# Performance work log

Hardware: AMD Instinct MI355X
Metric: run time of the kernel (lower is better)

## Reference

```python
import jax, jax.numpy as jnp
import numpy as np

STATE = 65536
INPUT = 32768
CONCAT = STATE + INPUT
H1, H2 = 100, 50
NGATES = 4  # forget, input, cell, output


def setup_inputs() -> dict:
    key = jax.random.key(0)
    ks = jax.random.split(key, 9)
    s = lambda n: 1.0 / np.sqrt(n)
    return {
        "cell_state_prev": jax.random.normal(ks[0], (STATE,), jnp.float32),
        "hypotesis": jax.random.normal(ks[1], (STATE,), jnp.float32),
        "x": jax.random.normal(ks[2], (INPUT,), jnp.float32),
        # stacked per-gate MLP params: gate order [forget, input, cell, output]
        "W1": jax.random.uniform(ks[3], (NGATES, H1, CONCAT), jnp.float32, -s(CONCAT), s(CONCAT)),
        "b1": jax.random.uniform(ks[4], (NGATES, H1), jnp.float32, -s(CONCAT), s(CONCAT)),
        "W2": jax.random.uniform(ks[5], (NGATES, H2, H1), jnp.float32, -s(H1), s(H1)),
        "b2": jax.random.uniform(ks[6], (NGATES, H2), jnp.float32, -s(H1), s(H1)),
        "W3": jax.random.uniform(ks[7], (NGATES, STATE, H2), jnp.float32, -s(H2), s(H2)),
        "b3": jax.random.uniform(ks[8], (NGATES, STATE), jnp.float32, -s(H2), s(H2)),
    }


def reference(cell_state_prev, hypotesis, x, W1, b1, W2, b2, W3, b3):
    c = jnp.concatenate([hypotesis, x])                     # [CONCAT]
    h1 = jax.nn.relu(jnp.einsum('ghc,c->gh', W1, c) + b1)   # [4, 100]
    h2 = jax.nn.relu(jnp.einsum('gkh,gh->gk', W2, h1) + b2) # [4, 50]
    z = jnp.einsum('gsk,gk->gs', W3, h2) + b3               # [4, STATE]
    forget_gate = jax.nn.sigmoid(z[0])
    input_gate = jax.nn.sigmoid(z[1])
    cell_state_hat = jnp.tanh(z[2])
    output_gate = jax.nn.sigmoid(z[3])
    new_cell_state = forget_gate * cell_state_prev + input_gate * cell_state_hat
    new_hypotesis = jnp.tanh(new_cell_state) * output_gate
    return (new_hypotesis, new_cell_state)
```

## Files before the change

kernel.cpp:

```cpp
#include <hip/hip_runtime.h>
#include <math.h>

#define STATE  65536
#define INPUT  32768
#define CONCAT 98304
#define H1_    100
#define H2_    50
#define NG     4

__global__ __launch_bounds__(1024) void k1_h1(
    const float* __restrict__ hyp, const float* __restrict__ x,
    const float* __restrict__ W1,  const float* __restrict__ b1,
    float* __restrict__ h1)
{
    const int row = blockIdx.x;
    const int tid = threadIdx.x;
    const float* __restrict__ Wrow = W1 + (size_t)row * CONCAT;

    float4 acc = make_float4(0.f, 0.f, 0.f, 0.f);

    #pragma unroll
    for (int it = 0; it < 16; ++it) {
        const int i = it * 4096 + tid * 4;
        const float4 w = *reinterpret_cast<const float4*>(Wrow + i);
        const float4 v = *reinterpret_cast<const float4*>(hyp + i);
        acc.x = fmaf(w.x, v.x, acc.x);
        acc.y = fmaf(w.y, v.y, acc.y);
        acc.z = fmaf(w.z, v.z, acc.z);
        acc.w = fmaf(w.w, v.w, acc.w);
    }
    #pragma unroll
    for (int it = 0; it < 8; ++it) {
        const int i = it * 4096 + tid * 4;
        const float4 w = *reinterpret_cast<const float4*>(Wrow + STATE + i);
        const float4 v = *reinterpret_cast<const float4*>(x + i);
        acc.x = fmaf(w.x, v.x, acc.x);
        acc.y = fmaf(w.y, v.y, acc.y);
        acc.z = fmaf(w.z, v.z, acc.z);
        acc.w = fmaf(w.w, v.w, acc.w);
    }

    float sum = (acc.x + acc.y) + (acc.z + acc.w);

    #pragma unroll
    for (int off = 32; off > 0; off >>= 1)
        sum += __shfl_down(sum, off, 64);

    __shared__ float wsum[16];
    if ((tid & 63) == 0) wsum[tid >> 6] = sum;
    __syncthreads();

    if (tid < 16) {
        float s = wsum[tid];
        s += __shfl_down(s, 8, 64);
        s += __shfl_down(s, 4, 64);
        s += __shfl_down(s, 2, 64);
        s += __shfl_down(s, 1, 64);
        if (tid == 0) h1[row] = fmaxf(s + b1[row], 0.f);
    }
}

__global__ __launch_bounds__(256) void k3_out(
    const float* __restrict__ h1, const float* __restrict__ W2,
    const float* __restrict__ b2, const float* __restrict__ W3,
    const float* __restrict__ b3, const float* __restrict__ cprev,
    float* __restrict__ out)
{
    __shared__ float h1s[NG * H1_];
    __shared__ float h2s[NG * H2_];
    __shared__ float zsh[NG * 64];

    const int tid = threadIdx.x;

    for (int i = tid; i < NG * H1_; i += 256) h1s[i] = h1[i];
    __syncthreads();

    if (tid < NG * H2_) {
        const int g = tid / H2_;
        const float* __restrict__ Wr = W2 + tid * H1_;
        float4 a = make_float4(0.f, 0.f, 0.f, 0.f);
        #pragma unroll
        for (int j = 0; j < H1_ / 4; ++j) {
            const float4 w = *reinterpret_cast<const float4*>(Wr + 4 * j);
            a.x = fmaf(w.x, h1s[g * H1_ + 4 * j + 0], a.x);
            a.y = fmaf(w.y, h1s[g * H1_ + 4 * j + 1], a.y);
            a.z = fmaf(w.z, h1s[g * H1_ + 4 * j + 2], a.z);
            a.w = fmaf(w.w, h1s[g * H1_ + 4 * j + 3], a.w);
        }
        const float v = (a.x + a.y) + (a.z + a.w) + b2[tid];
        h2s[tid] = fmaxf(v, 0.f);
    }
    __syncthreads();

    const int g    = tid >> 6;
    const int lane = tid & 63;
    const int s    = blockIdx.x * 64 + lane;
    const float* __restrict__ Wr = W3 + ((size_t)g * STATE + s) * H2_;
    float a0 = 0.f, a1 = 0.f;
    #pragma unroll
    for (int k = 0; k < H2_; k += 2) {
        const float2 w = *reinterpret_cast<const float2*>(Wr + k);
        a0 = fmaf(w.x, h2s[g * H2_ + k + 0], a0);
        a1 = fmaf(w.y, h2s[g * H2_ + k + 1], a1);
    }
    zsh[g * 64 + lane] = a0 + a1 + b3[(size_t)g * STATE + s];
    __syncthreads();

    if (tid < 64) {
        const int ss = blockIdx.x * 64 + tid;
        const float zf = zsh[0 * 64 + tid];
        const float zi = zsh[1 * 64 + tid];
        const float zc = zsh[2 * 64 + tid];
        const float zo = zsh[3 * 64 + tid];
        const float fg = 1.f / (1.f + expf(-zf));
        const float ig = 1.f / (1.f + expf(-zi));
        const float ch = tanhf(zc);
        const float og = 1.f / (1.f + expf(-zo));
        const float nc = fg * cprev[ss] + ig * ch;
        const float nh = tanhf(nc) * og;
        out[ss]         = nh;
        out[STATE + ss] = nc;
    }
}

extern "C" void kernel_launch(void* const* d_in, const int* in_sizes, int n_in,
                              void* d_out, int out_size, void* d_ws, size_t ws_size,
                              hipStream_t stream) {
    const float* cprev = (const float*)d_in[0];
    const float* hyp   = (const float*)d_in[1];
    const float* x     = (const float*)d_in[2];
    const float* W1    = (const float*)d_in[3];
    const float* b1    = (const float*)d_in[4];
    const float* W2    = (const float*)d_in[5];
    const float* b2    = (const float*)d_in[6];
    const float* W3    = (const float*)d_in[7];
    const float* b3    = (const float*)d_in[8];
    float* out = (float*)d_out;
    float* h1  = (float*)d_ws;

    k1_h1<<<NG * H1_, 1024, 0, stream>>>(hyp, x, W1, b1, h1);
    k3_out<<<STATE / 64, 256, 0, stream>>>(h1, W2, b2, W3, b3, cprev, out);
}
```

Before: 294.2 us.

## Split W1 GEMV rows into column segments with partial sums reduced downstream

```diff
diff --git a/kernel.cpp b/kernel.cpp
--- a/kernel.cpp
+++ b/kernel.cpp
@@ -1,78 +1,71 @@
 #include <hip/hip_runtime.h>
 #include <math.h>
 
-#define STATE  65536
-#define INPUT  32768
-#define CONCAT 98304
-#define H1_    100
-#define H2_    50
-#define NG     4
+#define STATE   65536
+#define INPUT   32768
+#define CONCAT  98304
+#define H1_     100
+#define H2_     50
+#define NG      4
+#define NROWS   (NG * H1_)
+#define SEGS    6
+#define SEGCOLS 16384
 
-__global__ __launch_bounds__(1024) void k1_h1(
+__global__ __launch_bounds__(256) void k1_partial(
     const float* __restrict__ hyp, const float* __restrict__ x,
-    const float* __restrict__ W1,  const float* __restrict__ b1,
-    float* __restrict__ h1)
+    const float* __restrict__ W1,  float* __restrict__ part)
 {
-    const int row = blockIdx.x;
+    const int bid = blockIdx.x;
+    const int seg = bid / NROWS;
+    const int row = bid - seg * NROWS;
     const int tid = threadIdx.x;
-    const float* __restrict__ Wrow = W1 + (size_t)row * CONCAT;
+
+    const float* __restrict__ vec =
+        (seg < 4) ? (hyp + seg * SEGCOLS) : (x + (seg - 4) * SEGCOLS);
+    const float* __restrict__ w = W1 + (size_t)row * CONCAT + seg * SEGCOLS;
 
     float4 acc = make_float4(0.f, 0.f, 0.f, 0.f);
-
     #pragma unroll
     for (int it = 0; it < 16; ++it) {
-        const int i = it * 4096 + tid * 4;
-        const float4 w = *reinterpret_cast<const float4*>(Wrow + i);
-        const float4 v = *reinterpret_cast<const float4*>(hyp + i);
-        acc.x = fmaf(w.x, v.x, acc.x);
-        acc.y = fmaf(w.y, v.y, acc.y);
-        acc.z = fmaf(w.z, v.z, acc.z);
-        acc.w = fmaf(w.w, v.w, acc.w);
+        const int i = it * 1024 + tid * 4;
+        const float4 wv = *reinterpret_cast<const float4*>(w + i);
+        const float4 vv = *reinterpret_cast<const float4*>(vec + i);
+        acc.x = fmaf(wv.x, vv.x, acc.x);
+        acc.y = fmaf(wv.y, vv.y, acc.y);
+        acc.z = fmaf(wv.z, vv.z, acc.z);
+        acc.w = fmaf(wv.w, vv.w, acc.w);
     }
-    #pragma unroll
-    for (int it = 0; it < 8; ++it) {
-        const int i = it * 4096 + tid * 4;
-        const float4 w = *reinterpret_cast<const float4*>(Wrow + STATE + i);
-        const float4 v = *reinterpret_cast<const float4*>(x + i);
-        acc.x = fmaf(w.x, v.x, acc.x);
-        acc.y = fmaf(w.y, v.y, acc.y);
-        acc.z = fmaf(w.z, v.z, acc.z);
-        acc.w = fmaf(w.w, v.w, acc.w);
-    }
-
     float sum = (acc.x + acc.y) + (acc.z + acc.w);
 
     #pragma unroll
     for (int off = 32; off > 0; off >>= 1)
         sum += __shfl_down(sum, off, 64);
 
-    __shared__ float wsum[16];
+    __shared__ float wsum[4];
     if ((tid & 63) == 0) wsum[tid >> 6] = sum;
     __syncthreads();
-
-    if (tid < 16) {
-        float s = wsum[tid];
-        s += __shfl_down(s, 8, 64);
-        s += __shfl_down(s, 4, 64);
-        s += __shfl_down(s, 2, 64);
-        s += __shfl_down(s, 1, 64);
-        if (tid == 0) h1[row] = fmaxf(s + b1[row], 0.f);
-    }
+    if (tid == 0)
+        part[bid] = (wsum[0] + wsum[1]) + (wsum[2] + wsum[3]);
 }
 
 __global__ __launch_bounds__(256) void k3_out(
-    const float* __restrict__ h1, const float* __restrict__ W2,
-    const float* __restrict__ b2, const float* __restrict__ W3,
-    const float* __restrict__ b3, const float* __restrict__ cprev,
-    float* __restrict__ out)
+    const float* __restrict__ part, const float* __restrict__ b1,
+    const float* __restrict__ W2,   const float* __restrict__ b2,
+    const float* __restrict__ W3,   const float* __restrict__ b3,
+    const float* __restrict__ cprev, float* __restrict__ out)
 {
-    __shared__ float h1s[NG * H1_];
+    __shared__ float h1s[NROWS];
     __shared__ float h2s[NG * H2_];
     __shared__ float zsh[NG * 64];
 
     const int tid = threadIdx.x;
 
-    for (int i = tid; i < NG * H1_; i += 256) h1s[i] = h1[i];
+    for (int i = tid; i < NROWS; i += 256) {
+        float s = b1[i];
+        #pragma unroll
+        for (int seg = 0; seg < SEGS; ++seg) s += part[seg * NROWS + i];
+        h1s[i] = fmaxf(s, 0.f);
+    }
     __syncthreads();
 
     if (tid < NG * H2_) {
@@ -135,9 +128,9 @@
     const float* b2    = (const float*)d_in[6];
     const float* W3    = (const float*)d_in[7];
     const float* b3    = (const float*)d_in[8];
-    float* out = (float*)d_out;
-    float* h1  = (float*)d_ws;
+    float* out  = (float*)d_out;
+    float* part = (float*)d_ws;
 
-    k1_h1<<<NG * H1_, 1024, 0, stream>>>(hyp, x, W1, b1, h1);
-    k3_out<<<STATE / 64, 256, 0, stream>>>(h1, W2, b2, W3, b3, cprev, out);
+    k1_partial<<<SEGS * NROWS, 256, 0, stream>>>(hyp, x, W1, part);
+    k3_out<<<STATE / 64, 256, 0, stream>>>(part, b1, W2, b2, W3, b3, cprev, out);
 }
```

New measurement: 285.2 us. 1.03x faster.
